# Performance work log

Measured on AMD Instinct MI355X. Metric: run time of the kernel, lower is better.

The kernel has to match this reference:

```python
import jax, jax.numpy as jnp
import numpy as np

HEADS = 8
# (src_type, dst_type) for the 8 edge types; node types: 0=op, 1=machine, 2=job
EDGE_DEFS = ((2, 0), (0, 2), (0, 0), (0, 0), (0, 1), (0, 1), (1, 0), (1, 0))
EPS = 1e-5


def _graph_norm(x, gamma, beta):
    # PyG LayerNorm(mode='graph') with batch=None: normalize over ALL nodes and features
    mu = x.mean()
    std = jnp.sqrt(((x - mu) ** 2).mean())
    return (x - mu) / (std + EPS) * gamma + beta


def _hgt_layer(xs, edges, Wkqv, bkqv, krel, vrel, prel, Wout, bout, skip):
    h = xs[0].shape[-1]
    D = h // HEADS
    Ns = [int(x.shape[0]) for x in xs]
    off = np.concatenate([[0], np.cumsum(Ns)])
    Ntot = int(off[-1])
    k, q, v = [], [], []
    for t, x in enumerate(xs):
        kqv = x @ Wkqv[t] + bkqv[t]                    # [N_t, 3h]
        kt, qt, vt = jnp.split(kqv, 3, axis=1)
        k.append(kt.reshape(-1, HEADS, D))
        q.append(qt.reshape(-1, HEADS, D))
        v.append(vt.reshape(-1, HEADS, D))
    alphas, msgs, idxs = [], [], []
    for e, (s, d) in enumerate(EDGE_DEFS):
        src, dst = edges[e][0], edges[e][1]
        # per-edge-type relation transform applied per source node, then gathered per edge
        ke = jnp.einsum('nhd,hde->nhe', k[s], krel[e])[src]   # [E, H, D]
        ve = jnp.einsum('nhd,hde->nhe', v[s], vrel[e])[src]   # [E, H, D]
        qe = q[d][dst]                                        # [E, H, D]
        a = (qe * ke).sum(-1) * prel[e] / jnp.sqrt(jnp.asarray(D, qe.dtype))  # [E, H]
        alphas.append(a)
        msgs.append(ve)
        idxs.append(dst + int(off[d]))
    alpha = jnp.concatenate(alphas, 0)
    msg = jnp.concatenate(msgs, 0)
    idx = jnp.concatenate(idxs, 0)
    # segment softmax over ALL incoming edges per (type-offset) destination node
    amax = jax.ops.segment_max(alpha, idx, num_segments=Ntot)
    ex = jnp.exp(alpha - amax[idx])
    den = jax.ops.segment_sum(ex, idx, num_segments=Ntot)
    w = ex / den[idx]
    agg = jax.ops.segment_sum(msg * w[..., None], idx, num_segments=Ntot).reshape(Ntot, h)
    outs = []
    for t in range(3):
        o = jax.nn.gelu(agg[off[t]:off[t + 1]], approximate=False) @ Wout[t] + bout[t]
        g = jax.nn.sigmoid(skip[t])
        outs.append(g * o + (1.0 - g) * xs[t])
    return outs


def _forward(op_x, machine_x, job_x, W_op, b_op, W_mach, b_mach, W_job, b_job,
             ln_gamma, ln_beta, Wkqv, bkqv, krel, vrel, prel, Wout, bout, skip,
             Wp1, bp1, Wp2, bp2, Wp3, bp3, Wv1, bv1, Wv2, bv2,
             edges, op_idx, m_idx):
    xs = [
        _graph_norm(op_x @ W_op + b_op, ln_gamma[0], ln_beta[0]),
        _graph_norm(machine_x @ W_mach + b_mach, ln_gamma[1], ln_beta[1]),
        _graph_norm(job_x @ W_job + b_job, ln_gamma[2], ln_beta[2]),
    ]
    for l in range(Wkqv.shape[0]):
        xs = _hgt_layer(xs, edges, Wkqv[l], bkqv[l], krel[l], vrel[l], prel[l],
                        Wout[l], bout[l], skip[l])
    op_e, mach_e, job_e = xs
    g = jnp.concatenate([op_e.mean(0), mach_e.mean(0), job_e.mean(0)])  # [3h] global pooled
    value = (jax.nn.relu(g @ Wv1 + bv1) @ Wv2 + bv2)[0]
    P = op_idx.shape[0]
    z = jnp.concatenate([op_e[op_idx], mach_e[m_idx],
                         jnp.broadcast_to(g, (P, g.shape[0]))], axis=1)   # [P, 5h]
    z = jax.nn.relu(z @ Wp1 + bp1)
    z = jax.nn.relu(z @ Wp2 + bp2)
    logits = (z @ Wp3 + bp3)[:, 0]
    return logits, value


def setup_inputs() -> dict:
    key = jax.random.key(0)
    ks = iter(jax.random.split(key, 64))
    NOP, NM, NJ = 50_000, 1_000, 5_000
    H, L, P = 64, 2, 20_000
    D = H // HEADS
    OPF, MF, JF = 8, 7, 7

    def nrm(shape, scale):
        return jax.random.normal(next(ks), shape, jnp.float32) * scale

    def edge(n_src, n_dst, E):
        src = jax.random.randint(next(ks), (E,), 0, n_src, jnp.int32)
        dst = jax.random.randint(next(ks), (E,), 0, n_dst, jnp.int32)
        return jnp.stack([src, dst])

    return {
        'op_x': nrm((NOP, OPF), 1.0),
        'machine_x': nrm((NM, MF), 1.0),
        'job_x': nrm((NJ, JF), 1.0),
        'W_op': nrm((OPF, H), OPF ** -0.5), 'b_op': jnp.zeros((H,), jnp.float32),
        'W_mach': nrm((MF, H), MF ** -0.5), 'b_mach': jnp.zeros((H,), jnp.float32),
        'W_job': nrm((JF, H), JF ** -0.5), 'b_job': jnp.zeros((H,), jnp.float32),
        'ln_gamma': jnp.ones((3, H), jnp.float32), 'ln_beta': jnp.zeros((3, H), jnp.float32),
        'Wkqv': nrm((L, 3, H, 3 * H), H ** -0.5), 'bkqv': jnp.zeros((L, 3, 3 * H), jnp.float32),
        'krel': nrm((L, 8, HEADS, D, D), D ** -0.5), 'vrel': nrm((L, 8, HEADS, D, D), D ** -0.5),
        'prel': jnp.ones((L, 8, HEADS), jnp.float32),
        'Wout': nrm((L, 3, H, H), H ** -0.5), 'bout': jnp.zeros((L, 3, H), jnp.float32),
        'skip': jnp.ones((L, 3), jnp.float32),
        'Wp1': nrm((5 * H, H), (5 * H) ** -0.5), 'bp1': jnp.zeros((H,), jnp.float32),
        'Wp2': nrm((H, H // 2), H ** -0.5), 'bp2': jnp.zeros((H // 2,), jnp.float32),
        'Wp3': nrm((H // 2, 1), (H // 2) ** -0.5), 'bp3': jnp.zeros((1,), jnp.float32),
        'Wv1': nrm((3 * H, H), (3 * H) ** -0.5), 'bv1': jnp.zeros((H,), jnp.float32),
        'Wv2': nrm((H, 1), H ** -0.5), 'bv2': jnp.zeros((1,), jnp.float32),
        'e_contains': edge(NJ, NOP, 50_000),
        'e_belongs': edge(NOP, NJ, 50_000),
        'e_prec': edge(NOP, NOP, 50_000),
        'e_mprec': edge(NOP, NOP, 50_000),
        'e_onmach': edge(NOP, NM, 50_000),
        'e_assign': edge(NOP, NM, 50_000),
        'e_canproc': edge(NM, NOP, 150_000),
        'e_proc': edge(NM, NOP, 50_000),
        'op_idx': jax.random.randint(next(ks), (P,), 0, NOP, jnp.int32),
        'm_idx': jax.random.randint(next(ks), (P,), 0, NM, jnp.int32),
    }


def reference(op_x, machine_x, job_x, W_op, b_op, W_mach, b_mach, W_job, b_job,
              ln_gamma, ln_beta, Wkqv, bkqv, krel, vrel, prel, Wout, bout, skip,
              Wp1, bp1, Wp2, bp2, Wp3, bp3, Wv1, bv1, Wv2, bv2,
              e_contains, e_belongs, e_prec, e_mprec, e_onmach, e_assign,
              e_canproc, e_proc, op_idx, m_idx):
    edges = (e_contains, e_belongs, e_prec, e_mprec, e_onmach, e_assign, e_canproc, e_proc)
    return _forward(op_x, machine_x, job_x, W_op, b_op, W_mach, b_mach, W_job, b_job,
                    ln_gamma, ln_beta, Wkqv, bkqv, krel, vrel, prel, Wout, bout, skip,
                    Wp1, bp1, Wp2, bp2, Wp3, bp3, Wv1, bv1, Wv2, bv2,
                    edges, op_idx, m_idx)
```

## Files before the change

### kernel.cpp

```cpp
#include <hip/hip_runtime.h>


#define KT 32
#define OT 64

__global__ void k_zero2(unsigned int* __restrict__ a, int na,
                        unsigned int* __restrict__ b, int nb) {
    int i = blockIdx.x * 256 + threadIdx.x;
    int st = gridDim.x * 256;
    int tot = na + nb;
    for (; i < tot; i += st) {
        if (i < na) a[i] = 0u; else b[i - na] = 0u;
    }
}

__global__ void k_build(const int* __restrict__ p0, const int* __restrict__ p1,
                        const int* __restrict__ p2, const int* __restrict__ p3,
                        const int* __restrict__ p4, const int* __restrict__ p5,
                        const int* __restrict__ p6, const int* __restrict__ p7,
                        int c1, int c2, int c3, int c4, int c5, int c6, int c7, int c8,
                        int* __restrict__ gdst, int* __restrict__ pack,
                        int* __restrict__ cnt, int fb,
                        const float* __restrict__ op_x, const float* __restrict__ mach_x,
                        const float* __restrict__ job_x,
                        const float* __restrict__ W_op, const float* __restrict__ b_op,
                        const float* __restrict__ W_mach, const float* __restrict__ b_mach,
                        const float* __restrict__ W_job, const float* __restrict__ b_job,
                        float* __restrict__ X, float* __restrict__ nacc,
                        int N0, int N1, int N2) {
    if (blockIdx.x < fb) {
        int g = blockIdx.x * 256 + threadIdx.x;
        if (g >= c8) return;
        const int* ep; int base, E0, et, soff, doff;
        int OJ = N0 + N1;
        if (g < c1)      { ep = p0; base = 0;  E0 = c1 - 0;  et = 0; soff = OJ;  doff = 0;  }
        else if (g < c2) { ep = p1; base = c1; E0 = c2 - c1; et = 1; soff = 0;   doff = OJ; }
        else if (g < c3) { ep = p2; base = c2; E0 = c3 - c2; et = 2; soff = 0;   doff = 0;  }
        else if (g < c4) { ep = p3; base = c3; E0 = c4 - c3; et = 3; soff = 0;   doff = 0;  }
        else if (g < c5) { ep = p4; base = c4; E0 = c5 - c4; et = 4; soff = 0;   doff = N0; }
        else if (g < c6) { ep = p5; base = c5; E0 = c6 - c5; et = 5; soff = 0;   doff = N0; }
        else if (g < c7) { ep = p6; base = c6; E0 = c7 - c6; et = 6; soff = N0;  doff = 0;  }
        else             { ep = p7; base = c7; E0 = c8 - c7; et = 7; soff = N0;  doff = 0;  }
        int i = g - base;
        int gd = ep[E0 + i] + doff;
        gdst[g] = gd;
        pack[g] = (ep[i] + soff) | (et << 24);
        atomicAdd(&cnt[gd], 1);
        return;
    }
    int bid = blockIdx.x - fb;
    int tid = threadIdx.x;
    int j = tid & 63, w = tid >> 6;
    float w0[8], w1[7], w2[7];
    for (int k = 0; k < 8; k++) w0[k] = W_op[k * 64 + j];
    for (int k = 0; k < 7; k++) w1[k] = W_mach[k * 64 + j];
    for (int k = 0; k < 7; k++) w2[k] = W_job[k * 64 + j];
    float b0 = b_op[j], b1 = b_mach[j], b2 = b_job[j];
    float s10 = 0, s20 = 0, s11 = 0, s21 = 0, s12 = 0, s22 = 0;
    int Ntot = N0 + N1 + N2;
    for (int n = bid * 4 + w; n < Ntot; n += 512 * 4) {
        float a;
        if (n < N0) {
            const float* xr = op_x + (size_t)n * 8;
            a = b0;
            for (int k = 0; k < 8; k++) a += xr[k] * w0[k];
            s10 += a; s20 += a * a;
        } else if (n < N0 + N1) {
            const float* xr = mach_x + (size_t)(n - N0) * 7;
            a = b1;
            for (int k = 0; k < 7; k++) a += xr[k] * w1[k];
            s11 += a; s21 += a * a;
        } else {
            const float* xr = job_x + (size_t)(n - N0 - N1) * 7;
            a = b2;
            for (int k = 0; k < 7; k++) a += xr[k] * w2[k];
            s12 += a; s22 += a * a;
        }
        X[(size_t)n * 64 + j] = a;
    }
    for (int o = 32; o > 0; o >>= 1) {
        s10 += __shfl_down(s10, o); s20 += __shfl_down(s20, o);
        s11 += __shfl_down(s11, o); s21 += __shfl_down(s21, o);
        s12 += __shfl_down(s12, o); s22 += __shfl_down(s22, o);
    }
    __shared__ float r[4][6];
    if (j == 0) {
        r[w][0] = s10; r[w][1] = s20; r[w][2] = s11;
        r[w][3] = s21; r[w][4] = s12; r[w][5] = s22;
    }
    __syncthreads();
    if (tid < 6) {
        float v = r[0][tid] + r[1][tid] + r[2][tid] + r[3][tid];
        atomicAdd(&nacc[tid], v);
    }
}

__global__ void k_scan1(const int* __restrict__ cnt, int* __restrict__ partial, int Ntot) {
    __shared__ int s[256];
    int t = threadIdx.x;
    int i = blockIdx.x * 256 + t;
    s[t] = (i < Ntot) ? cnt[i] : 0;
    __syncthreads();
    for (int o = 128; o > 0; o >>= 1) {
        if (t < o) s[t] += s[t + o];
        __syncthreads();
    }
    if (t == 0) partial[blockIdx.x] = s[0];
}

__global__ void k_scan2(const int* __restrict__ cnt, const int* __restrict__ partial,
                        int* __restrict__ rowptr, int* __restrict__ cursor,
                        int Ntot, int Etot) {
    __shared__ int s[256];
    __shared__ int pbase;
    int t = threadIdx.x;
    int ps = 0;
    for (int c = t; c < blockIdx.x; c += 256) ps += partial[c];
    s[t] = ps;
    __syncthreads();
    for (int o = 128; o > 0; o >>= 1) {
        if (t < o) s[t] += s[t + o];
        __syncthreads();
    }
    if (t == 0) pbase = s[0];
    __syncthreads();
    int base = pbase;
    int i = blockIdx.x * 256 + t;
    int v = (i < Ntot) ? cnt[i] : 0;
    s[t] = v;
    __syncthreads();
    for (int off = 1; off < 256; off <<= 1) {
        int add = (t >= off) ? s[t - off] : 0;
        __syncthreads();
        s[t] += add;
        __syncthreads();
    }
    if (i < Ntot) {
        int r = base + s[t] - v;
        rowptr[i] = r;
        cursor[i] = r;
    }
    if (blockIdx.x == 0 && t == 0) rowptr[Ntot] = Etot;
}

__global__ void k_scatter(const int* __restrict__ gdst, const int* __restrict__ pack,
                          int* __restrict__ cursor, int* __restrict__ csr, int Etot) {
    int i = blockIdx.x * 256 + threadIdx.x;
    if (i >= Etot) return;
    int d = gdst[i];
    int pos = atomicAdd(&cursor[d], 1);
    csr[pos] = pack[i];
}

__global__ void k_kqvT(float* __restrict__ X, const float* __restrict__ nacc,
                       const float* __restrict__ ln_gamma, const float* __restrict__ ln_beta,
                       const float* __restrict__ Wl, const float* __restrict__ bl,
                       float* __restrict__ KQV, int tb0, int tb1,
                       int N0, int N1, int N2, int do_norm) {
    __shared__ float Ws[64 * 192];
    __shared__ float Xs[64 * 36];
    __shared__ float Bs[192];
    int b = blockIdx.x;
    int t, nbase, Nt, chunk;
    if (b < tb0)            { t = 0; chunk = b;             nbase = 0;       Nt = N0; }
    else if (b < tb0 + tb1) { t = 1; chunk = b - tb0;       nbase = N0;      Nt = N1; }
    else                    { t = 2; chunk = b - tb0 - tb1; nbase = N0 + N1; Nt = N2; }
    int n0 = nbase + chunk * KT;
    int cntm = nbase + Nt - n0; if (cntm > KT) cntm = KT;

    int tid = threadIdx.x;
    const float* W = Wl + (size_t)t * 64 * 192;
    for (int i = tid; i < 64 * 192; i += 192) Ws[i] = W[i];
    Bs[tid] = bl[t * 192 + tid];

    float mu = 0.0f, sc = 0.0f;
    if (do_norm) {
        float inv = 1.0f / ((float)Nt * 64.0f);
        mu = nacc[2 * t] * inv;
        float var = nacc[2 * t + 1] * inv - mu * mu;
        sc = 1.0f / (sqrtf(fmaxf(var, 0.0f)) + 1e-5f);
    }
    for (int idx = tid; idx < KT * 64; idx += 192) {
        int m = idx >> 6, k = idx & 63;
        float v = 0.0f;
        if (m < cntm) {
            v = X[(size_t)(n0 + m) * 64 + k];
            if (do_norm) {
                v = (v - mu) * sc * ln_gamma[t * 64 + k] + ln_beta[t * 64 + k];
                X[(size_t)(n0 + m) * 64 + k] = v;
            }
        }
        Xs[k * 36 + m] = v;
    }
    __syncthreads();

    int c = tid;
    float bc = Bs[c];
    float acc[KT];
#pragma unroll
    for (int m = 0; m < KT; m++) acc[m] = bc;
    for (int k = 0; k < 64; k++) {
        float wv = Ws[k * 192 + c];
        const float4* xr = (const float4*)(Xs + k * 36);
#pragma unroll
        for (int q = 0; q < KT / 4; q++) {
            float4 x4 = xr[q];
            acc[q * 4 + 0] += x4.x * wv;
            acc[q * 4 + 1] += x4.y * wv;
            acc[q * 4 + 2] += x4.z * wv;
            acc[q * 4 + 3] += x4.w * wv;
        }
    }
    for (int m = 0; m < cntm; m++)
        KQV[(size_t)(n0 + m) * 192 + c] = acc[m];
}

__global__ void k_attnagg(const float* __restrict__ KQV, const int* __restrict__ csr,
                          const int* __restrict__ rowptr,
                          const float* __restrict__ krel_l, const float* __restrict__ vrel_l,
                          const float* __restrict__ prel_l, float* __restrict__ agg, int Ntot) {
    __shared__ float KRs[8 * 8 * 72];
    __shared__ float VRs[8 * 8 * 72];
    int tid = threadIdx.x;
    for (int i = tid; i < 4096; i += 512) {
        int eth = i >> 6, rest = i & 63;
        KRs[eth * 72 + rest] = krel_l[i] * (prel_l[eth] * 0.35355339059327373f);
        VRs[eth * 72 + rest] = vrel_l[i];
    }
    __syncthreads();

    int j = tid & 63, h = j >> 3, ee = j & 7;
    int wave  = blockIdx.x * 8 + (tid >> 6);
    int nwave = gridDim.x * 8;
    for (int n = wave; n < Ntot; n += nwave) {
        float qv = KQV[(size_t)n * 192 + 64 + j];
        float num = 0.0f, den = 0.0f;
        int e0 = rowptr[n], e1 = rowptr[n + 1];
        int idx = e0;
        for (; idx + 2 <= e1; idx += 2) {
            int pk0 = csr[idx], pk1 = csr[idx + 1];
            int sn0 = pk0 & 0xFFFFFF, et0 = ((unsigned int)pk0) >> 24;
            int sn1 = pk1 & 0xFFFFFF, et1 = ((unsigned int)pk1) >> 24;
            const float4* ka = (const float4*)(KQV + (size_t)sn0 * 192 + h * 8);
            const float4* va = (const float4*)(KQV + (size_t)sn0 * 192 + 128 + h * 8);
            const float4* kb = (const float4*)(KQV + (size_t)sn1 * 192 + h * 8);
            const float4* vb = (const float4*)(KQV + (size_t)sn1 * 192 + 128 + h * 8);
            float4 a0 = ka[0], a1 = ka[1], av0 = va[0], av1 = va[1];
            float4 b0 = kb[0], b1 = kb[1], bv0 = vb[0], bv1 = vb[1];
            const float* KR0 = KRs + (et0 * 8 + h) * 72 + ee;
            const float* VR0 = VRs + (et0 * 8 + h) * 72 + ee;
            const float* KR1 = KRs + (et1 * 8 + h) * 72 + ee;
            const float* VR1 = VRs + (et1 * 8 + h) * 72 + ee;
            float ke0 = a0.x * KR0[0]  + a0.y * KR0[8]  + a0.z * KR0[16] + a0.w * KR0[24]
                      + a1.x * KR0[32] + a1.y * KR0[40] + a1.z * KR0[48] + a1.w * KR0[56];
            float ve0 = av0.x * VR0[0]  + av0.y * VR0[8]  + av0.z * VR0[16] + av0.w * VR0[24]
                      + av1.x * VR0[32] + av1.y * VR0[40] + av1.z * VR0[48] + av1.w * VR0[56];
            float ke1 = b0.x * KR1[0]  + b0.y * KR1[8]  + b0.z * KR1[16] + b0.w * KR1[24]
                      + b1.x * KR1[32] + b1.y * KR1[40] + b1.z * KR1[48] + b1.w * KR1[56];
            float ve1 = bv0.x * VR1[0]  + bv0.y * VR1[8]  + bv0.z * VR1[16] + bv0.w * VR1[24]
                      + bv1.x * VR1[32] + bv1.y * VR1[40] + bv1.z * VR1[48] + bv1.w * VR1[56];
            float t0 = qv * ke0;
            t0 += __shfl_xor(t0, 1); t0 += __shfl_xor(t0, 2); t0 += __shfl_xor(t0, 4);
            float t1 = qv * ke1;
            t1 += __shfl_xor(t1, 1); t1 += __shfl_xor(t1, 2); t1 += __shfl_xor(t1, 4);
            float ex0 = __expf(t0);
            float ex1 = __expf(t1);
            num += ex0 * ve0 + ex1 * ve1;
            den += ex0 + ex1;
        }
        if (idx < e1) {
            int pk = csr[idx];
            int sn = pk & 0xFFFFFF, et = ((unsigned int)pk) >> 24;
            const float4* kr4 = (const float4*)(KQV + (size_t)sn * 192 + h * 8);
            const float4* vr4 = (const float4*)(KQV + (size_t)sn * 192 + 128 + h * 8);
            float4 k0 = kr4[0], k1 = kr4[1], v0 = vr4[0], v1 = vr4[1];
            const float* KR = KRs + (et * 8 + h) * 72 + ee;
            const float* VR = VRs + (et * 8 + h) * 72 + ee;
            float ke = k0.x * KR[0]  + k0.y * KR[8]  + k0.z * KR[16] + k0.w * KR[24]
                     + k1.x * KR[32] + k1.y * KR[40] + k1.z * KR[48] + k1.w * KR[56];
            float ve = v0.x * VR[0]  + v0.y * VR[8]  + v0.z * VR[16] + v0.w * VR[24]
                     + v1.x * VR[32] + v1.y * VR[40] + v1.z * VR[48] + v1.w * VR[56];
            float tq = qv * ke;
            tq += __shfl_xor(tq, 1); tq += __shfl_xor(tq, 2); tq += __shfl_xor(tq, 4);
            float ex = __expf(tq);
            num += ex * ve;
            den += ex;
        }
        agg[(size_t)n * 64 + j] = (den > 0.0f) ? (num / den) : 0.0f;
    }
}

__global__ void k_outT(const float* __restrict__ agg, float* __restrict__ X,
                       const float* __restrict__ Wl, const float* __restrict__ bl,
                       const float* __restrict__ skipl, float* __restrict__ gsum,
                       int tb0, int tb1, int N0, int N1, int N2, int do_pool) {
    __shared__ float Ws[64 * 64];
    __shared__ float Gs[64 * 68];
    int b = blockIdx.x;
    int t, nbase, Nt, chunk;
    if (b < tb0)            { t = 0; chunk = b;             nbase = 0;       Nt = N0; }
    else if (b < tb0 + tb1) { t = 1; chunk = b - tb0;       nbase = N0;      Nt = N1; }
    else                    { t = 2; chunk = b - tb0 - tb1; nbase = N0 + N1; Nt = N2; }
    int n0 = nbase + chunk * OT;
    int cntm = nbase + Nt - n0; if (cntm > OT) cntm = OT;

    int tid = threadIdx.x;
    const float* W = Wl + (size_t)t * 64 * 64;
    for (int i = tid; i < 4096; i += 256) Ws[i] = W[i];
    for (int idx = tid; idx < OT * 64; idx += 256) {
        int m = idx >> 6, k = idx & 63;
        float v = 0.0f;
        if (m < cntm) {
            float x = agg[(size_t)(n0 + m) * 64 + k];
            v = 0.5f * x * (1.0f + erff(x * 0.70710678118654752f));
        }
        Gs[k * 68 + m] = v;
    }
    __syncthreads();

    int c = tid & 63, w = tid >> 6;
    float bc = bl[t * 64 + c];
    float gk = 1.0f / (1.0f + __expf(-skipl[t]));
    int m0 = w * 16;
    float acc[16];
#pragma unroll
    for (int i = 0; i < 16; i++) acc[i] = bc;
    for (int k = 0; k < 64; k++) {
        float wv = Ws[k * 64 + c];
        const float4* gr = (const float4*)(Gs + k * 68 + m0);
#pragma unroll
        for (int q = 0; q < 4; q++) {
            float4 g4 = gr[q];
            acc[q * 4 + 0] += g4.x * wv;
            acc[q * 4 + 1] += g4.y * wv;
            acc[q * 4 + 2] += g4.z * wv;
            acc[q * 4 + 3] += g4.w * wv;
        }
    }
    float psum = 0.0f;
    for (int i = 0; i < 16; i++) {
        int m = m0 + i;
        if (m < cntm) {
            float xold = X[(size_t)(n0 + m) * 64 + c];
            float xn = gk * acc[i] + (1.0f - gk) * xold;
            X[(size_t)(n0 + m) * 64 + c] = xn;
            psum += xn;
        }
    }
    if (do_pool) {
        __syncthreads();
        Gs[w * 64 + c] = psum;
        __syncthreads();
        if (tid < 64) {
            float tot = Gs[c] + Gs[64 + c] + Gs[128 + c] + Gs[192 + c];
            atomicAdd(&gsum[t * 64 + c], tot);
        }
    }
}

__global__ void HGTPolicy_53051436040798_kernel(
        const float* __restrict__ X, const float* __restrict__ gsum,
        const int* __restrict__ op_idx, const int* __restrict__ m_idx,
        const float* __restrict__ Wp1, const float* __restrict__ bp1,
        const float* __restrict__ Wp2, const float* __restrict__ bp2,
        const float* __restrict__ Wp3, const float* __restrict__ bp3,
        const float* __restrict__ Wv1, const float* __restrict__ bv1,
        const float* __restrict__ Wv2, const float* __restrict__ bv2,
        float* __restrict__ out, int N0, int N1, int N2, int P, int nb) {
    int tid = threadIdx.x;
    if (blockIdx.x == nb) {
        __shared__ float g[192];
        __shared__ float h1[64];
        int j = tid;
        if (j < 192) {
            float Nd = (j < 64) ? (float)N0 : ((j < 128) ? (float)N1 : (float)N2);
            g[j] = gsum[j] / Nd;
        }
        __syncthreads();
        if (j < 64) {
            float a = bv1[j];
            for (int k = 0; k < 192; k++) a += g[k] * Wv1[k * 64 + j];
            h1[j] = fmaxf(a, 0.0f);
        }
        __syncthreads();
        if (j == 0) {
            float v = bv2[0];
            for (int k = 0; k < 64; k++) v += h1[k] * Wv2[k];
            out[P] = v;
        }
        return;
    }
    __shared__ float z[8][320];
    __shared__ float h1p[8][64];
    __shared__ float h2p[8][32];
    int pp = tid >> 6, j = tid & 63;
    int p = blockIdx.x * 8 + pp;
    int valid = (p < P);
    if (valid) {
        int on = op_idx[p], mn = m_idx[p];
        z[pp][j]       = X[(size_t)on * 64 + j];
        z[pp][64 + j]  = X[(size_t)(N0 + mn) * 64 + j];
        z[pp][128 + j] = gsum[j] / (float)N0;
        z[pp][192 + j] = gsum[64 + j] / (float)N1;
        z[pp][256 + j] = gsum[128 + j] / (float)N2;
    }
    __syncthreads();
    if (valid) {
        const float* zp = z[pp];
        float a = bp1[j];
        for (int k = 0; k < 320; k++) a += zp[k] * Wp1[k * 64 + j];
        h1p[pp][j] = fmaxf(a, 0.0f);
    }
    __syncthreads();
    if (valid && j < 32) {
        const float* hp = h1p[pp];
        float a2 = bp2[j];
        for (int k = 0; k < 64; k++) a2 += hp[k] * Wp2[k * 32 + j];
        h2p[pp][j] = fmaxf(a2, 0.0f);
    }
    __syncthreads();
    if (valid && j == 0) {
        const float* hp = h2p[pp];
        float lg = bp3[0];
        for (int k = 0; k < 32; k++) lg += hp[k] * Wp3[k];
        out[p] = lg;
    }
}

extern "C" void kernel_launch(void* const* d_in, const int* in_sizes, int n_in,
                              void* d_out, int out_size, void* d_ws, size_t ws_size,
                              hipStream_t stream) {
    const float* op_x      = (const float*)d_in[0];
    const float* machine_x = (const float*)d_in[1];
    const float* job_x     = (const float*)d_in[2];
    const float* W_op   = (const float*)d_in[3];
    const float* b_op   = (const float*)d_in[4];
    const float* W_mach = (const float*)d_in[5];
    const float* b_mach = (const float*)d_in[6];
    const float* W_job  = (const float*)d_in[7];
    const float* b_job  = (const float*)d_in[8];
    const float* ln_gamma = (const float*)d_in[9];
    const float* ln_beta  = (const float*)d_in[10];
    const float* Wkqv = (const float*)d_in[11];
    const float* bkqv = (const float*)d_in[12];
    const float* krel = (const float*)d_in[13];
    const float* vrel = (const float*)d_in[14];
    const float* prel = (const float*)d_in[15];
    const float* Wout = (const float*)d_in[16];
    const float* bout = (const float*)d_in[17];
    const float* skip = (const float*)d_in[18];
    const float* Wp1 = (const float*)d_in[19];
    const float* bp1 = (const float*)d_in[20];
    const float* Wp2 = (const float*)d_in[21];
    const float* bp2 = (const float*)d_in[22];
    const float* Wp3 = (const float*)d_in[23];
    const float* bp3 = (const float*)d_in[24];
    const float* Wv1 = (const float*)d_in[25];
    const float* bv1 = (const float*)d_in[26];
    const float* Wv2 = (const float*)d_in[27];
    const float* bv2 = (const float*)d_in[28];
    const int* op_idx = (const int*)d_in[37];
    const int* m_idx  = (const int*)d_in[38];

    const int NOP = in_sizes[0] / 8;
    const int NM  = in_sizes[1] / 7;
    const int NJ  = in_sizes[2] / 7;
    const int L   = in_sizes[11] / (3 * 64 * 192);
    const int P   = in_sizes[37];
    const int Ntot = NOP + NM + NJ;

    const int* eptr[8];
    int eoff[9];
    eoff[0] = 0;
    for (int e = 0; e < 8; e++) {
        eptr[e] = (const int*)d_in[29 + e];
        eoff[e + 1] = eoff[e] + in_sizes[29 + e] / 2;
    }
    const int Etot = eoff[8];

    float* ws = (float*)d_ws;
    size_t o = 0;
    float* X    = ws + o; o += (size_t)Ntot * 64;
    float* KQV  = ws + o; o += (size_t)Ntot * 192;
    float* agg  = ws + o; o += (size_t)Ntot * 64;
    float* gsum = ws + o; o += 192;
    float* nacc = ws + o; o += 8;
    int* ib     = (int*)(ws + o);
    size_t io = 0;
    int* cnt    = ib + io; io += Ntot;
    int* rowptr = ib + io; io += Ntot + 1;
    int* cursor = ib + io; io += Ntot;
    int* partial= ib + io; io += 1024;
    int* gdst   = ib + io; io += Etot;
    int* packs  = ib + io; io += Etot;
    int* csr    = ib + io; io += Etot;

    const int kb0 = (NOP + KT - 1) / KT, kb1 = (NM + KT - 1) / KT, kb2 = (NJ + KT - 1) / KT;
    const int kgrid = kb0 + kb1 + kb2;
    const int ob0 = (NOP + OT - 1) / OT, ob1 = (NM + OT - 1) / OT, ob2 = (NJ + OT - 1) / OT;
    const int ogrid = ob0 + ob1 + ob2;
    const int nchunks = (Ntot + 255) / 256;
    const int fb = (Etot + 255) / 256;

    k_zero2<<<64, 256, 0, stream>>>((unsigned int*)cnt, Ntot, (unsigned int*)gsum, 200);

    k_build<<<fb + 512, 256, 0, stream>>>(
        eptr[0], eptr[1], eptr[2], eptr[3], eptr[4], eptr[5], eptr[6], eptr[7],
        eoff[1], eoff[2], eoff[3], eoff[4], eoff[5], eoff[6], eoff[7], eoff[8],
        gdst, packs, cnt, fb,
        op_x, machine_x, job_x, W_op, b_op, W_mach, b_mach, W_job, b_job,
        X, nacc, NOP, NM, NJ);

    k_scan1<<<nchunks, 256, 0, stream>>>(cnt, partial, Ntot);
    k_scan2<<<nchunks, 256, 0, stream>>>(cnt, partial, rowptr, cursor, Ntot, Etot);
    k_scatter<<<(Etot + 255) / 256, 256, 0, stream>>>(gdst, packs, cursor, csr, Etot);

    for (int l = 0; l < L; l++) {
        k_kqvT<<<kgrid, 192, 0, stream>>>(X, nacc, ln_gamma, ln_beta,
                                          Wkqv + (size_t)l * 3 * 64 * 192,
                                          bkqv + (size_t)l * 3 * 192,
                                          KQV, kb0, kb1, NOP, NM, NJ, (l == 0) ? 1 : 0);
        k_attnagg<<<1024, 512, 0, stream>>>(KQV, csr, rowptr,
                                            krel + (size_t)l * 4096,
                                            vrel + (size_t)l * 4096,
                                            prel + (size_t)l * 64,
                                            agg, Ntot);
        k_outT<<<ogrid, 256, 0, stream>>>(agg, X,
                                          Wout + (size_t)l * 3 * 64 * 64,
                                          bout + (size_t)l * 3 * 64,
                                          skip + (size_t)l * 3,
                                          gsum, ob0, ob1, NOP, NM, NJ,
                                          (l + 1 == L) ? 1 : 0);
    }

    const int nbP = (P + 7) / 8;
    HGTPolicy_53051436040798_kernel<<<nbP + 1, 512, 0, stream>>>(
        X, gsum, op_idx, m_idx, Wp1, bp1, Wp2, bp2, Wp3, bp3,
        Wv1, bv1, Wv2, bv2, (float*)d_out, NOP, NM, NJ, P, nbP);
}
```

Baseline: 669.2 us.

## Bucket CSR edges by destination and edge type to hoist relation weights

The CSR is now keyed by (destination, edge type), with 8 row pointers per node, so each type's edges sit together. The attention kernel loops over the 8 types per destination and loads that type's krel/vrel column into registers once, instead of reading shared memory for every edge. The packed source index no longer carries the edge type. In exchange the count, scan and cursor arrays are 8x larger, the scan kernels do more work, and each node reads 9 row-pointer entries.

Measured after the change: 674.1 us. About the same (+0.7%).

```diff
diff --git a/kernel.cpp b/kernel.cpp
--- a/kernel.cpp
+++ b/kernel.cpp
@@ -19,7 +19,7 @@
                         const int* __restrict__ p4, const int* __restrict__ p5,
                         const int* __restrict__ p6, const int* __restrict__ p7,
                         int c1, int c2, int c3, int c4, int c5, int c6, int c7, int c8,
-                        int* __restrict__ gdst, int* __restrict__ pack,
+                        int* __restrict__ gkey, int* __restrict__ pack,
                         int* __restrict__ cnt, int fb,
                         const float* __restrict__ op_x, const float* __restrict__ mach_x,
                         const float* __restrict__ job_x,
@@ -42,10 +42,10 @@
         else if (g < c7) { ep = p6; base = c6; E0 = c7 - c6; et = 6; soff = N0;  doff = 0;  }
         else             { ep = p7; base = c7; E0 = c8 - c7; et = 7; soff = N0;  doff = 0;  }
         int i = g - base;
-        int gd = ep[E0 + i] + doff;
-        gdst[g] = gd;
-        pack[g] = (ep[i] + soff) | (et << 24);
-        atomicAdd(&cnt[gd], 1);
+        int kd = (ep[E0 + i] + doff) * 8 + et;
+        gkey[g] = kd;
+        pack[g] = ep[i] + soff;
+        atomicAdd(&cnt[kd], 1);
         return;
     }
     int bid = blockIdx.x - fb;
@@ -95,11 +95,11 @@
     }
 }
 
-__global__ void k_scan1(const int* __restrict__ cnt, int* __restrict__ partial, int Ntot) {
+__global__ void k_scan1(const int* __restrict__ cnt, int* __restrict__ partial, int M) {
     __shared__ int s[256];
     int t = threadIdx.x;
     int i = blockIdx.x * 256 + t;
-    s[t] = (i < Ntot) ? cnt[i] : 0;
+    s[t] = (i < M) ? cnt[i] : 0;
     __syncthreads();
     for (int o = 128; o > 0; o >>= 1) {
         if (t < o) s[t] += s[t + o];
@@ -109,8 +109,8 @@
 }
 
 __global__ void k_scan2(const int* __restrict__ cnt, const int* __restrict__ partial,
-                        int* __restrict__ rowptr, int* __restrict__ cursor,
-                        int Ntot, int Etot) {
+                        int* __restrict__ rowptr8, int* __restrict__ cursor,
+                        int M, int Etot) {
     __shared__ int s[256];
     __shared__ int pbase;
     int t = threadIdx.x;
@@ -126,7 +126,7 @@
     __syncthreads();
     int base = pbase;
     int i = blockIdx.x * 256 + t;
-    int v = (i < Ntot) ? cnt[i] : 0;
+    int v = (i < M) ? cnt[i] : 0;
     s[t] = v;
     __syncthreads();
     for (int off = 1; off < 256; off <<= 1) {
@@ -135,19 +135,19 @@
         s[t] += add;
         __syncthreads();
     }
-    if (i < Ntot) {
+    if (i < M) {
         int r = base + s[t] - v;
-        rowptr[i] = r;
+        rowptr8[i] = r;
         cursor[i] = r;
     }
-    if (blockIdx.x == 0 && t == 0) rowptr[Ntot] = Etot;
-}
-
-__global__ void k_scatter(const int* __restrict__ gdst, const int* __restrict__ pack,
+    if (blockIdx.x == 0 && t == 0) rowptr8[M] = Etot;
+}
+
+__global__ void k_scatter(const int* __restrict__ gkey, const int* __restrict__ pack,
                           int* __restrict__ cursor, int* __restrict__ csr, int Etot) {
     int i = blockIdx.x * 256 + threadIdx.x;
     if (i >= Etot) return;
-    int d = gdst[i];
+    int d = gkey[i];
     int pos = atomicAdd(&cursor[d], 1);
     csr[pos] = pack[i];
 }
@@ -216,7 +216,7 @@
 }
 
 __global__ void k_attnagg(const float* __restrict__ KQV, const int* __restrict__ csr,
-                          const int* __restrict__ rowptr,
+                          const int* __restrict__ rowptr8,
                           const float* __restrict__ krel_l, const float* __restrict__ vrel_l,
                           const float* __restrict__ prel_l, float* __restrict__ agg, int Ntot) {
     __shared__ float KRs[8 * 8 * 72];
@@ -235,56 +235,59 @@
     for (int n = wave; n < Ntot; n += nwave) {
         float qv = KQV[(size_t)n * 192 + 64 + j];
         float num = 0.0f, den = 0.0f;
-        int e0 = rowptr[n], e1 = rowptr[n + 1];
-        int idx = e0;
-        for (; idx + 2 <= e1; idx += 2) {
-            int pk0 = csr[idx], pk1 = csr[idx + 1];
-            int sn0 = pk0 & 0xFFFFFF, et0 = ((unsigned int)pk0) >> 24;
-            int sn1 = pk1 & 0xFFFFFF, et1 = ((unsigned int)pk1) >> 24;
-            const float4* ka = (const float4*)(KQV + (size_t)sn0 * 192 + h * 8);
-            const float4* va = (const float4*)(KQV + (size_t)sn0 * 192 + 128 + h * 8);
-            const float4* kb = (const float4*)(KQV + (size_t)sn1 * 192 + h * 8);
-            const float4* vb = (const float4*)(KQV + (size_t)sn1 * 192 + 128 + h * 8);
-            float4 a0 = ka[0], a1 = ka[1], av0 = va[0], av1 = va[1];
-            float4 b0 = kb[0], b1 = kb[1], bv0 = vb[0], bv1 = vb[1];
-            const float* KR0 = KRs + (et0 * 8 + h) * 72 + ee;
-            const float* VR0 = VRs + (et0 * 8 + h) * 72 + ee;
-            const float* KR1 = KRs + (et1 * 8 + h) * 72 + ee;
-            const float* VR1 = VRs + (et1 * 8 + h) * 72 + ee;
-            float ke0 = a0.x * KR0[0]  + a0.y * KR0[8]  + a0.z * KR0[16] + a0.w * KR0[24]
-                      + a1.x * KR0[32] + a1.y * KR0[40] + a1.z * KR0[48] + a1.w * KR0[56];
-            float ve0 = av0.x * VR0[0]  + av0.y * VR0[8]  + av0.z * VR0[16] + av0.w * VR0[24]
-                      + av1.x * VR0[32] + av1.y * VR0[40] + av1.z * VR0[48] + av1.w * VR0[56];
-            float ke1 = b0.x * KR1[0]  + b0.y * KR1[8]  + b0.z * KR1[16] + b0.w * KR1[24]
-                      + b1.x * KR1[32] + b1.y * KR1[40] + b1.z * KR1[48] + b1.w * KR1[56];
-            float ve1 = bv0.x * VR1[0]  + bv0.y * VR1[8]  + bv0.z * VR1[16] + bv0.w * VR1[24]
-                      + bv1.x * VR1[32] + bv1.y * VR1[40] + bv1.z * VR1[48] + bv1.w * VR1[56];
-            float t0 = qv * ke0;
-            t0 += __shfl_xor(t0, 1); t0 += __shfl_xor(t0, 2); t0 += __shfl_xor(t0, 4);
-            float t1 = qv * ke1;
-            t1 += __shfl_xor(t1, 1); t1 += __shfl_xor(t1, 2); t1 += __shfl_xor(t1, 4);
-            float ex0 = __expf(t0);
-            float ex1 = __expf(t1);
-            num += ex0 * ve0 + ex1 * ve1;
-            den += ex0 + ex1;
-        }
-        if (idx < e1) {
-            int pk = csr[idx];
-            int sn = pk & 0xFFFFFF, et = ((unsigned int)pk) >> 24;
-            const float4* kr4 = (const float4*)(KQV + (size_t)sn * 192 + h * 8);
-            const float4* vr4 = (const float4*)(KQV + (size_t)sn * 192 + 128 + h * 8);
-            float4 k0 = kr4[0], k1 = kr4[1], v0 = vr4[0], v1 = vr4[1];
-            const float* KR = KRs + (et * 8 + h) * 72 + ee;
-            const float* VR = VRs + (et * 8 + h) * 72 + ee;
-            float ke = k0.x * KR[0]  + k0.y * KR[8]  + k0.z * KR[16] + k0.w * KR[24]
-                     + k1.x * KR[32] + k1.y * KR[40] + k1.z * KR[48] + k1.w * KR[56];
-            float ve = v0.x * VR[0]  + v0.y * VR[8]  + v0.z * VR[16] + v0.w * VR[24]
-                     + v1.x * VR[32] + v1.y * VR[40] + v1.z * VR[48] + v1.w * VR[56];
-            float tq = qv * ke;
-            tq += __shfl_xor(tq, 1); tq += __shfl_xor(tq, 2); tq += __shfl_xor(tq, 4);
-            float ex = __expf(tq);
-            num += ex * ve;
-            den += ex;
+        int e0 = rowptr8[n * 8];
+        for (int et = 0; et < 8; et++) {
+            int e1 = rowptr8[n * 8 + et + 1];
+            if (e0 < e1) {
+                const float* KR = KRs + (et * 8 + h) * 72 + ee;
+                const float* VR = VRs + (et * 8 + h) * 72 + ee;
+                float kr0 = KR[0],  kr1 = KR[8],  kr2 = KR[16], kr3 = KR[24];
+                float kr4 = KR[32], kr5 = KR[40], kr6 = KR[48], kr7 = KR[56];
+                float vr0 = VR[0],  vr1 = VR[8],  vr2 = VR[16], vr3 = VR[24];
+                float vr4 = VR[32], vr5 = VR[40], vr6 = VR[48], vr7 = VR[56];
+                int idx = e0;
+                for (; idx + 2 <= e1; idx += 2) {
+                    int sn0 = csr[idx], sn1 = csr[idx + 1];
+                    const float4* ka = (const float4*)(KQV + (size_t)sn0 * 192 + h * 8);
+                    const float4* va = (const float4*)(KQV + (size_t)sn0 * 192 + 128 + h * 8);
+                    const float4* kb = (const float4*)(KQV + (size_t)sn1 * 192 + h * 8);
+                    const float4* vb = (const float4*)(KQV + (size_t)sn1 * 192 + 128 + h * 8);
+                    float4 a0 = ka[0], a1 = ka[1], av0 = va[0], av1 = va[1];
+                    float4 b0 = kb[0], b1 = kb[1], bv0 = vb[0], bv1 = vb[1];
+                    float ke0 = a0.x * kr0 + a0.y * kr1 + a0.z * kr2 + a0.w * kr3
+                              + a1.x * kr4 + a1.y * kr5 + a1.z * kr6 + a1.w * kr7;
+                    float ve0 = av0.x * vr0 + av0.y * vr1 + av0.z * vr2 + av0.w * vr3
+                              + av1.x * vr4 + av1.y * vr5 + av1.z * vr6 + av1.w * vr7;
+                    float ke1 = b0.x * kr0 + b0.y * kr1 + b0.z * kr2 + b0.w * kr3
+                              + b1.x * kr4 + b1.y * kr5 + b1.z * kr6 + b1.w * kr7;
+                    float ve1 = bv0.x * vr0 + bv0.y * vr1 + bv0.z * vr2 + bv0.w * vr3
+                              + bv1.x * vr4 + bv1.y * vr5 + bv1.z * vr6 + bv1.w * vr7;
+                    float t0 = qv * ke0;
+                    t0 += __shfl_xor(t0, 1); t0 += __shfl_xor(t0, 2); t0 += __shfl_xor(t0, 4);
+                    float t1 = qv * ke1;
+                    t1 += __shfl_xor(t1, 1); t1 += __shfl_xor(t1, 2); t1 += __shfl_xor(t1, 4);
+                    float ex0 = __expf(t0);
+                    float ex1 = __expf(t1);
+                    num += ex0 * ve0 + ex1 * ve1;
+                    den += ex0 + ex1;
+                }
+                if (idx < e1) {
+                    int sn = csr[idx];
+                    const float4* kr4p = (const float4*)(KQV + (size_t)sn * 192 + h * 8);
+                    const float4* vr4p = (const float4*)(KQV + (size_t)sn * 192 + 128 + h * 8);
+                    float4 k0 = kr4p[0], k1 = kr4p[1], v0 = vr4p[0], v1 = vr4p[1];
+                    float ke = k0.x * kr0 + k0.y * kr1 + k0.z * kr2 + k0.w * kr3
+                             + k1.x * kr4 + k1.y * kr5 + k1.z * kr6 + k1.w * kr7;
+                    float ve = v0.x * vr0 + v0.y * vr1 + v0.z * vr2 + v0.w * vr3
+                             + v1.x * vr4 + v1.y * vr5 + v1.z * vr6 + v1.w * vr7;
+                    float tq = qv * ke;
+                    tq += __shfl_xor(tq, 1); tq += __shfl_xor(tq, 2); tq += __shfl_xor(tq, 4);
+                    float ex = __expf(tq);
+                    num += ex * ve;
+                    den += ex;
+                }
+            }
+            e0 = e1;
         }
         agg[(size_t)n * 64 + j] = (den > 0.0f) ? (num / den) : 0.0f;
     }
@@ -468,6 +471,7 @@
     const int L   = in_sizes[11] / (3 * 64 * 192);
     const int P   = in_sizes[37];
     const int Ntot = NOP + NM + NJ;
+    const int M = Ntot * 8;
 
     const int* eptr[8];
     int eoff[9];
@@ -487,40 +491,40 @@
     float* nacc = ws + o; o += 8;
     int* ib     = (int*)(ws + o);
     size_t io = 0;
-    int* cnt    = ib + io; io += Ntot;
-    int* rowptr = ib + io; io += Ntot + 1;
-    int* cursor = ib + io; io += Ntot;
-    int* partial= ib + io; io += 1024;
-    int* gdst   = ib + io; io += Etot;
-    int* packs  = ib + io; io += Etot;
-    int* csr    = ib + io; io += Etot;
+    int* cnt     = ib + io; io += M;
+    int* rowptr8 = ib + io; io += M + 1;
+    int* cursor  = ib + io; io += M;
+    int* partial = ib + io; io += 2048;
+    int* gkey    = ib + io; io += Etot;
+    int* packs   = ib + io; io += Etot;
+    int* csr     = ib + io; io += Etot;
 
     const int kb0 = (NOP + KT - 1) / KT, kb1 = (NM + KT - 1) / KT, kb2 = (NJ + KT - 1) / KT;
     const int kgrid = kb0 + kb1 + kb2;
     const int ob0 = (NOP + OT - 1) / OT, ob1 = (NM + OT - 1) / OT, ob2 = (NJ + OT - 1) / OT;
     const int ogrid = ob0 + ob1 + ob2;
-    const int nchunks = (Ntot + 255) / 256;
+    const int nchunks = (M + 255) / 256;
     const int fb = (Etot + 255) / 256;
 
-    k_zero2<<<64, 256, 0, stream>>>((unsigned int*)cnt, Ntot, (unsigned int*)gsum, 200);
+    k_zero2<<<256, 256, 0, stream>>>((unsigned int*)cnt, M, (unsigned int*)gsum, 200);
 
     k_build<<<fb + 512, 256, 0, stream>>>(
         eptr[0], eptr[1], eptr[2], eptr[3], eptr[4], eptr[5], eptr[6], eptr[7],
         eoff[1], eoff[2], eoff[3], eoff[4], eoff[5], eoff[6], eoff[7], eoff[8],
-        gdst, packs, cnt, fb,
+        gkey, packs, cnt, fb,
         op_x, machine_x, job_x, W_op, b_op, W_mach, b_mach, W_job, b_job,
         X, nacc, NOP, NM, NJ);
 
-    k_scan1<<<nchunks, 256, 0, stream>>>(cnt, partial, Ntot);
-    k_scan2<<<nchunks, 256, 0, stream>>>(cnt, partial, rowptr, cursor, Ntot, Etot);
-    k_scatter<<<(Etot + 255) / 256, 256, 0, stream>>>(gdst, packs, cursor, csr, Etot);
+    k_scan1<<<nchunks, 256, 0, stream>>>(cnt, partial, M);
+    k_scan2<<<nchunks, 256, 0, stream>>>(cnt, partial, rowptr8, cursor, M, Etot);
+    k_scatter<<<(Etot + 255) / 256, 256, 0, stream>>>(gkey, packs, cursor, csr, Etot);
 
     for (int l = 0; l < L; l++) {
         k_kqvT<<<kgrid, 192, 0, stream>>>(X, nacc, ln_gamma, ln_beta,
                                           Wkqv + (size_t)l * 3 * 64 * 192,
                                           bkqv + (size_t)l * 3 * 192,
                                           KQV, kb0, kb1, NOP, NM, NJ, (l == 0) ? 1 : 0);
-        k_attnagg<<<1024, 512, 0, stream>>>(KQV, csr, rowptr,
+        k_attnagg<<<1024, 512, 0, stream>>>(KQV, csr, rowptr8,
                                             krel + (size_t)l * 4096,
                                             vrel + (size_t)l * 4096,
                                             prel + (size_t)l * 64,
```
